# Kernel tuning notes

Measured on AMD Instinct MI355X. Metric: run time of the kernel, lower is better.

The kernel has to match this reference:

```python
import jax, jax.numpy as jnp
import numpy as np


def setup_inputs() -> dict:
    key = jax.random.key(0)
    kq, kk, kv = jax.random.split(key, 3)
    B, N, H, D = 1, 4096, 16, 64
    q = jax.random.normal(kq, (B, N, H, D), dtype=jnp.float32)
    k = jax.random.normal(kk, (B, N, H, D), dtype=jnp.float32)
    v = jax.random.normal(kv, (B, N, H, D), dtype=jnp.float32)
    return {"q": q, "k": k, "v": v}


def reference(q, k, v):
    # q, k, v: [b, n, h, d]
    d = q.shape[-1]
    scale = 1.0 / jnp.sqrt(jnp.asarray(d, dtype=q.dtype))
    # scores: [b, h, n_q, n_k]
    scores = jnp.einsum("bqhd,bkhd->bhqk", q, k) * scale
    attn = jax.nn.softmax(scores, axis=-1)
    # output back in [b, n, h, d] layout
    out = jnp.einsum("bhqk,bkhd->bqhd", attn, v)
    return out
```

## Files before the change

kernel.cpp:

```cpp
#include <hip/hip_runtime.h>
#include <hip/hip_bf16.h>

#define H 16
#define D 64
#define NSEQ 4096
#define BM 128
#define BN 64
#define NT (NSEQ / BN)

typedef __attribute__((ext_vector_type(8))) short bf16x8;
typedef __attribute__((ext_vector_type(4))) short short4v;
typedef __attribute__((ext_vector_type(4))) float f32x4;
typedef __attribute__((ext_vector_type(4))) float f4v;

union BF8 { bf16x8 v; unsigned u[4]; };
union S4  { short4v s; unsigned u[2]; };

static __device__ __forceinline__ unsigned pk2(float lo, float hi) {
    __hip_bfloat162 h = __float22bfloat162_rn(float2{lo, hi});
    unsigned u;
    __builtin_memcpy(&u, &h, 4);
    return u;
}

static __device__ __forceinline__ float fexp2(float x) {
#if __has_builtin(__builtin_amdgcn_exp2f)
    return __builtin_amdgcn_exp2f(x);
#else
    return exp2f(x);
#endif
}

#define TO_GBL(p) ((const __attribute__((address_space(1))) int*)(unsigned long long)(p))
#define TO_LDS(p) ((__attribute__((address_space(3))) int*)(unsigned int)(unsigned long long)(p))

__global__ void prep(const float* __restrict__ k, const float* __restrict__ v,
                     short* __restrict__ kb, short* __restrict__ vt) {
    __shared__ short L[64 * 72];
    const int h = blockIdx.y, n0 = blockIdx.x * 64, t = threadIdx.x;
    const int rw = t >> 4, c4 = (t & 15) * 4;
    #pragma unroll
    for (int it = 0; it < 4; ++it) {
        const int row = rw + it * 16;
        const size_t gro = ((size_t)(n0 + row) * H + h) * D + c4;
        f4v kf = *(const f4v*)(k + gro);
        S4 ks;
        ks.u[0] = pk2(kf[0], kf[1]);
        ks.u[1] = pk2(kf[2], kf[3]);
        *(short4v*)(kb + ((size_t)h * NSEQ + n0 + row) * D + c4) = ks.s;

        f4v vf = *(const f4v*)(v + gro);
        S4 vs;
        vs.u[0] = pk2(vf[0], vf[1]);
        vs.u[1] = pk2(vf[2], vf[3]);
        *(short4v*)&L[row * 72 + c4] = vs.s;
    }
    __syncthreads();
    const int tr = t & 15, tc = t >> 4;
    const int r0 = tr * 4, d0 = tc * 4;
    short4v ra[4];
    #pragma unroll
    for (int i = 0; i < 4; ++i) {
        const int s = r0 + i, s32 = s & 31, base32 = (s >> 5) * 32;
        const int phys = base32 + ((s32 >> 3) * 4 + (s32 & 3) + 16 * ((s32 >> 2) & 1));
        ra[i] = *(const short4v*)&L[phys * 72 + d0];
    }
    #pragma unroll
    for (int jj = 0; jj < 4; ++jj) {
        short4v o4 = (short4v){ra[0][jj], ra[1][jj], ra[2][jj], ra[3][jj]};
        *(short4v*)(vt + ((size_t)(h * D + d0 + jj)) * NSEQ + n0 + r0) = o4;
    }
}

__global__ __launch_bounds__(256, 2)
void attn_fwd(const float* __restrict__ q, const short* __restrict__ kb,
              const short* __restrict__ vtb, float* __restrict__ out)
{
    const int lin   = blockIdx.x;
    const int idx   = lin >> 3;
    const int h     = (lin & 7) * 2 + (idx >> 5);
    const int qbase = (idx & 31) * BM;

    const int tid   = threadIdx.x;
    const int wave  = tid >> 6;
    const int lane  = tid & 63;
    const int lm    = lane & 15;
    const int quad  = lane >> 4;
    const int sw    = lm & 7;

    __shared__ short Kt[4][BN * D];
    __shared__ short Vt[4][BN * D];

    const float c1 = 0.18033688011112042f;

    bf16x8 bq[2][2];
    #pragma unroll
    for (int g = 0; g < 2; ++g) {
        const int qrow = qbase + wave * 32 + g * 16 + lm;
        #pragma unroll
        for (int kc = 0; kc < 2; ++kc) {
            const float* qp = q + ((size_t)qrow * H + h) * D + kc * 32 + quad * 8;
            f4v q0 = *(const f4v*)qp;
            f4v q1 = *(const f4v*)(qp + 4);
            BF8 b;
            b.u[0] = pk2(q0[0] * c1, q0[1] * c1); b.u[1] = pk2(q0[2] * c1, q0[3] * c1);
            b.u[2] = pk2(q1[0] * c1, q1[1] * c1); b.u[3] = pk2(q1[2] * c1, q1[3] * c1);
            bq[g][kc] = b.v;
        }
    }

    BF8 ones;
    ones.u[0] = ones.u[1] = ones.u[2] = ones.u[3] = 0x3F803F80u;

    const f32x4 fz = (f32x4){0.f, 0.f, 0.f, 0.f};
    f32x4 o[2][4];
    #pragma unroll
    for (int g = 0; g < 2; ++g)
        #pragma unroll
        for (int mb = 0; mb < 4; ++mb) o[g][mb] = fz;
    f32x4 lacc[2];
    lacc[0] = fz; lacc[1] = fz;

    const int ci0 = (wave * 2 + 0) * 64 + lane;
    const int ci1 = (wave * 2 + 1) * 64 + lane;
    const int kr0 = ci0 >> 3, kp0 = (ci0 & 7) ^ (kr0 & 7);
    const int kr1 = ci1 >> 3, kp1 = (ci1 & 7) ^ (kr1 & 7);

    const short* kh = kb  + (size_t)h * NSEQ * D;
    const short* vh = vtb + (size_t)h * D * NSEQ;
    const short* pkA = kh + (size_t)kr0 * D + kp0 * 8;
    const short* pkB = kh + (size_t)kr1 * D + kp1 * 8;
    const short* pvA = vh + (size_t)kr0 * NSEQ + kp0 * 8;
    const short* pvB = vh + (size_t)kr1 * NSEQ + kp1 * 8;

    auto issue = [&](int b) {
        __builtin_amdgcn_global_load_lds(TO_GBL(pkA), TO_LDS(&Kt[b][(wave * 2 + 0) * 512]), 16, 0, 0);
        __builtin_amdgcn_global_load_lds(TO_GBL(pkB), TO_LDS(&Kt[b][(wave * 2 + 1) * 512]), 16, 0, 0);
        __builtin_amdgcn_global_load_lds(TO_GBL(pvA), TO_LDS(&Vt[b][(wave * 2 + 0) * 512]), 16, 0, 0);
        __builtin_amdgcn_global_load_lds(TO_GBL(pvB), TO_LDS(&Vt[b][(wave * 2 + 1) * 512]), 16, 0, 0);
        pkA += BN * D; pkB += BN * D; pvA += BN; pvB += BN;
    };

    const int posK0 = ((0 + quad) ^ sw) * 8;
    const int posK1 = ((4 + quad) ^ sw) * 8;

    auto compute = [&](int b) {
        const short* K_ = Kt[b];
        const short* V_ = Vt[b];
        f32x4 st[2][4];

        #pragma unroll
        for (int nb = 0; nb < 4; ++nb) {
            bf16x8 kf0 = *(const bf16x8*)&K_[(nb * 16 + lm) * 64 + posK0];
            bf16x8 kf1 = *(const bf16x8*)&K_[(nb * 16 + lm) * 64 + posK1];
            #pragma unroll
            for (int g = 0; g < 2; ++g) {
                st[g][nb] = __builtin_amdgcn_mfma_f32_16x16x32_bf16(kf0, bq[g][0], fz, 0, 0, 0);
                st[g][nb] = __builtin_amdgcn_mfma_f32_16x16x32_bf16(kf1, bq[g][1], st[g][nb], 0, 0, 0);
            }
        }

        #pragma unroll
        for (int g = 0; g < 2; ++g)
            #pragma unroll
            for (int nb = 0; nb < 4; ++nb)
                #pragma unroll
                for (int r = 0; r < 4; ++r)
                    st[g][nb][r] = fexp2(st[g][nb][r]);

        BF8 pb[2][2];
        #pragma unroll
        for (int g = 0; g < 2; ++g)
            #pragma unroll
            for (int c = 0; c < 2; ++c) {
                pb[g][c].u[0] = pk2(st[g][2 * c][0],     st[g][2 * c][1]);
                pb[g][c].u[1] = pk2(st[g][2 * c][2],     st[g][2 * c][3]);
                pb[g][c].u[2] = pk2(st[g][2 * c + 1][0], st[g][2 * c + 1][1]);
                pb[g][c].u[3] = pk2(st[g][2 * c + 1][2], st[g][2 * c + 1][3]);
            }

        #pragma unroll
        for (int g = 0; g < 2; ++g) {
            lacc[g] = __builtin_amdgcn_mfma_f32_16x16x32_bf16(ones.v, pb[g][0].v, lacc[g], 0, 0, 0);
            lacc[g] = __builtin_amdgcn_mfma_f32_16x16x32_bf16(ones.v, pb[g][1].v, lacc[g], 0, 0, 0);
        }

        #pragma unroll
        for (int c = 0; c < 2; ++c) {
            const int pos = ((c * 4 + quad) ^ sw) * 8;
            #pragma unroll
            for (int mb = 0; mb < 4; ++mb) {
                bf16x8 vf = *(const bf16x8*)&V_[(mb * 16 + lm) * 64 + pos];
                #pragma unroll
                for (int g = 0; g < 2; ++g)
                    o[g][mb] = __builtin_amdgcn_mfma_f32_16x16x32_bf16(vf, pb[g][c].v, o[g][mb], 0, 0, 0);
            }
        }
    };

#define WAITV0 asm volatile("s_waitcnt vmcnt(0)" ::: "memory")
#define BARRIER() do { __builtin_amdgcn_s_barrier(); asm volatile("" ::: "memory"); } while (0)

    issue(0); issue(1);

    for (int k = 0; k < 15; ++k) {
        WAITV0; BARRIER();
        issue(2); issue(3);
        compute(0); compute(1);
        WAITV0; BARRIER();
        issue(0); issue(1);
        compute(2); compute(3);
    }
    WAITV0; BARRIER();
    issue(2); issue(3);
    compute(0); compute(1);
    WAITV0; BARRIER();
    compute(2); compute(3);

    #pragma unroll
    for (int g = 0; g < 2; ++g) {
        const float inv = 1.0f / lacc[g][0];
        const int qrow = qbase + wave * 32 + g * 16 + lm;
        float* op = out + ((size_t)qrow * H + h) * D + quad * 4;
        #pragma unroll
        for (int mb = 0; mb < 4; ++mb) {
            f4v w;
            #pragma unroll
            for (int r = 0; r < 4; ++r) w[r] = o[g][mb][r] * inv;
            *(f4v*)(op + mb * 16) = w;
        }
    }
}

extern "C" void kernel_launch(void* const* d_in, const int* in_sizes, int n_in,
                              void* d_out, int out_size, void* d_ws, size_t ws_size,
                              hipStream_t stream) {
    const float* q = (const float*)d_in[0];
    const float* k = (const float*)d_in[1];
    const float* v = (const float*)d_in[2];
    float* out = (float*)d_out;

    short* kb = (short*)d_ws;
    short* vt = kb + (size_t)H * NSEQ * D;

    prep<<<dim3(NSEQ / 64, H), dim3(256), 0, stream>>>(k, v, kb, vt);
    attn_fwd<<<dim3((NSEQ / BM) * H), dim3(256), 0, stream>>>(q, kb, vt, out);
}
```

Before: 165.7 us.

## Use two waves per block with 64 query rows each for K/V fragment reuse

Shrinks the attention block from four waves to two, so each wave now handles 64 query rows (four 16-row groups) instead of 32. Each K and V fragment read from LDS is reused across twice as many MFMAs, and the K fragments are loaded once per tile up front. Each wave now issues twice as many global-to-LDS loads, the per-thread accumulator and register footprint roughly doubles, and there are fewer waves per block to hide latency. Launch bounds change to 128 threads with a minimum of one block.

After: 179.2 us. 1.08x slower.

```diff
diff --git a/kernel.cpp b/kernel.cpp
--- a/kernel.cpp
+++ b/kernel.cpp
@@ -72,7 +72,7 @@
     }
 }
 
-__global__ __launch_bounds__(256, 2)
+__global__ __launch_bounds__(128, 1)
 void attn_fwd(const float* __restrict__ q, const short* __restrict__ kb,
               const short* __restrict__ vtb, float* __restrict__ out)
 {
@@ -93,10 +93,10 @@
 
     const float c1 = 0.18033688011112042f;
 
-    bf16x8 bq[2][2];
-    #pragma unroll
-    for (int g = 0; g < 2; ++g) {
-        const int qrow = qbase + wave * 32 + g * 16 + lm;
+    bf16x8 bq[4][2];
+    #pragma unroll
+    for (int g = 0; g < 4; ++g) {
+        const int qrow = qbase + wave * 64 + g * 16 + lm;
         #pragma unroll
         for (int kc = 0; kc < 2; ++kc) {
             const float* qp = q + ((size_t)qrow * H + h) * D + kc * 32 + quad * 8;
@@ -113,32 +113,46 @@
     ones.u[0] = ones.u[1] = ones.u[2] = ones.u[3] = 0x3F803F80u;
 
     const f32x4 fz = (f32x4){0.f, 0.f, 0.f, 0.f};
-    f32x4 o[2][4];
-    #pragma unroll
-    for (int g = 0; g < 2; ++g)
+    f32x4 o[4][4];
+    #pragma unroll
+    for (int g = 0; g < 4; ++g)
         #pragma unroll
         for (int mb = 0; mb < 4; ++mb) o[g][mb] = fz;
-    f32x4 lacc[2];
-    lacc[0] = fz; lacc[1] = fz;
-
-    const int ci0 = (wave * 2 + 0) * 64 + lane;
-    const int ci1 = (wave * 2 + 1) * 64 + lane;
-    const int kr0 = ci0 >> 3, kp0 = (ci0 & 7) ^ (kr0 & 7);
-    const int kr1 = ci1 >> 3, kp1 = (ci1 & 7) ^ (kr1 & 7);
+    f32x4 lacc[4];
+    lacc[0] = fz; lacc[1] = fz; lacc[2] = fz; lacc[3] = fz;
+
+    const int cset = wave * 4;
+    const int ciA = (cset + 0) * 64 + lane;
+    const int ciB = (cset + 1) * 64 + lane;
+    const int ciC = (cset + 2) * 64 + lane;
+    const int ciD = (cset + 3) * 64 + lane;
+    const int krA = ciA >> 3, kpA = (ciA & 7) ^ (krA & 7);
+    const int krB = ciB >> 3, kpB = (ciB & 7) ^ (krB & 7);
+    const int krC = ciC >> 3, kpC = (ciC & 7) ^ (krC & 7);
+    const int krD = ciD >> 3, kpD = (ciD & 7) ^ (krD & 7);
 
     const short* kh = kb  + (size_t)h * NSEQ * D;
     const short* vh = vtb + (size_t)h * D * NSEQ;
-    const short* pkA = kh + (size_t)kr0 * D + kp0 * 8;
-    const short* pkB = kh + (size_t)kr1 * D + kp1 * 8;
-    const short* pvA = vh + (size_t)kr0 * NSEQ + kp0 * 8;
-    const short* pvB = vh + (size_t)kr1 * NSEQ + kp1 * 8;
+    const short* pkA = kh + (size_t)krA * D + kpA * 8;
+    const short* pkB = kh + (size_t)krB * D + kpB * 8;
+    const short* pkC = kh + (size_t)krC * D + kpC * 8;
+    const short* pkD = kh + (size_t)krD * D + kpD * 8;
+    const short* pvA = vh + (size_t)krA * NSEQ + kpA * 8;
+    const short* pvB = vh + (size_t)krB * NSEQ + kpB * 8;
+    const short* pvC = vh + (size_t)krC * NSEQ + kpC * 8;
+    const short* pvD = vh + (size_t)krD * NSEQ + kpD * 8;
 
     auto issue = [&](int b) {
-        __builtin_amdgcn_global_load_lds(TO_GBL(pkA), TO_LDS(&Kt[b][(wave * 2 + 0) * 512]), 16, 0, 0);
-        __builtin_amdgcn_global_load_lds(TO_GBL(pkB), TO_LDS(&Kt[b][(wave * 2 + 1) * 512]), 16, 0, 0);
-        __builtin_amdgcn_global_load_lds(TO_GBL(pvA), TO_LDS(&Vt[b][(wave * 2 + 0) * 512]), 16, 0, 0);
-        __builtin_amdgcn_global_load_lds(TO_GBL(pvB), TO_LDS(&Vt[b][(wave * 2 + 1) * 512]), 16, 0, 0);
-        pkA += BN * D; pkB += BN * D; pvA += BN; pvB += BN;
+        __builtin_amdgcn_global_load_lds(TO_GBL(pkA), TO_LDS(&Kt[b][(cset + 0) * 512]), 16, 0, 0);
+        __builtin_amdgcn_global_load_lds(TO_GBL(pkB), TO_LDS(&Kt[b][(cset + 1) * 512]), 16, 0, 0);
+        __builtin_amdgcn_global_load_lds(TO_GBL(pkC), TO_LDS(&Kt[b][(cset + 2) * 512]), 16, 0, 0);
+        __builtin_amdgcn_global_load_lds(TO_GBL(pkD), TO_LDS(&Kt[b][(cset + 3) * 512]), 16, 0, 0);
+        __builtin_amdgcn_global_load_lds(TO_GBL(pvA), TO_LDS(&Vt[b][(cset + 0) * 512]), 16, 0, 0);
+        __builtin_amdgcn_global_load_lds(TO_GBL(pvB), TO_LDS(&Vt[b][(cset + 1) * 512]), 16, 0, 0);
+        __builtin_amdgcn_global_load_lds(TO_GBL(pvC), TO_LDS(&Vt[b][(cset + 2) * 512]), 16, 0, 0);
+        __builtin_amdgcn_global_load_lds(TO_GBL(pvD), TO_LDS(&Vt[b][(cset + 3) * 512]), 16, 0, 0);
+        pkA += BN * D; pkB += BN * D; pkC += BN * D; pkD += BN * D;
+        pvA += BN; pvB += BN; pvC += BN; pvD += BN;
     };
 
     const int posK0 = ((0 + quad) ^ sw) * 8;
@@ -147,43 +161,42 @@
     auto compute = [&](int b) {
         const short* K_ = Kt[b];
         const short* V_ = Vt[b];
-        f32x4 st[2][4];
-
+
+        bf16x8 kf0[4], kf1[4];
         #pragma unroll
         for (int nb = 0; nb < 4; ++nb) {
-            bf16x8 kf0 = *(const bf16x8*)&K_[(nb * 16 + lm) * 64 + posK0];
-            bf16x8 kf1 = *(const bf16x8*)&K_[(nb * 16 + lm) * 64 + posK1];
-            #pragma unroll
-            for (int g = 0; g < 2; ++g) {
-                st[g][nb] = __builtin_amdgcn_mfma_f32_16x16x32_bf16(kf0, bq[g][0], fz, 0, 0, 0);
-                st[g][nb] = __builtin_amdgcn_mfma_f32_16x16x32_bf16(kf1, bq[g][1], st[g][nb], 0, 0, 0);
+            kf0[nb] = *(const bf16x8*)&K_[(nb * 16 + lm) * 64 + posK0];
+            kf1[nb] = *(const bf16x8*)&K_[(nb * 16 + lm) * 64 + posK1];
+        }
+
+        BF8 pb[4][2];
+        #pragma unroll
+        for (int g = 0; g < 4; ++g) {
+            f32x4 st[4];
+            #pragma unroll
+            for (int nb = 0; nb < 4; ++nb) {
+                st[nb] = __builtin_amdgcn_mfma_f32_16x16x32_bf16(kf0[nb], bq[g][0], fz, 0, 0, 0);
+                st[nb] = __builtin_amdgcn_mfma_f32_16x16x32_bf16(kf1[nb], bq[g][1], st[nb], 0, 0, 0);
             }
-        }
-
-        #pragma unroll
-        for (int g = 0; g < 2; ++g)
             #pragma unroll
             for (int nb = 0; nb < 4; ++nb)
                 #pragma unroll
                 for (int r = 0; r < 4; ++r)
-                    st[g][nb][r] = fexp2(st[g][nb][r]);
-
-        BF8 pb[2][2];
-        #pragma unroll
-        for (int g = 0; g < 2; ++g)
+                    st[nb][r] = fexp2(st[nb][r]);
             #pragma unroll
             for (int c = 0; c < 2; ++c) {
-                pb[g][c].u[0] = pk2(st[g][2 * c][0],     st[g][2 * c][1]);
-                pb[g][c].u[1] = pk2(st[g][2 * c][2],     st[g][2 * c][3]);
-                pb[g][c].u[2] = pk2(st[g][2 * c + 1][0], st[g][2 * c + 1][1]);
-                pb[g][c].u[3] = pk2(st[g][2 * c + 1][2], st[g][2 * c + 1][3]);
+                pb[g][c].u[0] = pk2(st[2 * c][0],     st[2 * c][1]);
+                pb[g][c].u[1] = pk2(st[2 * c][2],     st[2 * c][3]);
+                pb[g][c].u[2] = pk2(st[2 * c + 1][0], st[2 * c + 1][1]);
+                pb[g][c].u[3] = pk2(st[2 * c + 1][2], st[2 * c + 1][3]);
             }
-
-        #pragma unroll
-        for (int g = 0; g < 2; ++g) {
-            lacc[g] = __builtin_amdgcn_mfma_f32_16x16x32_bf16(ones.v, pb[g][0].v, lacc[g], 0, 0, 0);
-            lacc[g] = __builtin_amdgcn_mfma_f32_16x16x32_bf16(ones.v, pb[g][1].v, lacc[g], 0, 0, 0);
-        }
+        }
+
+        #pragma unroll
+        for (int c = 0; c < 2; ++c)
+            #pragma unroll
+            for (int g = 0; g < 4; ++g)
+                lacc[g] = __builtin_amdgcn_mfma_f32_16x16x32_bf16(ones.v, pb[g][c].v, lacc[g], 0, 0, 0);
 
         #pragma unroll
         for (int c = 0; c < 2; ++c) {
@@ -192,7 +205,7 @@
             for (int mb = 0; mb < 4; ++mb) {
                 bf16x8 vf = *(const bf16x8*)&V_[(mb * 16 + lm) * 64 + pos];
                 #pragma unroll
-                for (int g = 0; g < 2; ++g)
+                for (int g = 0; g < 4; ++g)
                     o[g][mb] = __builtin_amdgcn_mfma_f32_16x16x32_bf16(vf, pb[g][c].v, o[g][mb], 0, 0, 0);
             }
         }
@@ -218,9 +231,9 @@
     compute(2); compute(3);
 
     #pragma unroll
-    for (int g = 0; g < 2; ++g) {
+    for (int g = 0; g < 4; ++g) {
         const float inv = 1.0f / lacc[g][0];
-        const int qrow = qbase + wave * 32 + g * 16 + lm;
+        const int qrow = qbase + wave * 64 + g * 16 + lm;
         float* op = out + ((size_t)qrow * H + h) * D + quad * 4;
         #pragma unroll
         for (int mb = 0; mb < 4; ++mb) {
@@ -244,5 +257,5 @@
     short* vt = kb + (size_t)H * NSEQ * D;
 
     prep<<<dim3(NSEQ / 64, H), dim3(256), 0, stream>>>(k, v, kb, vt);
-    attn_fwd<<<dim3((NSEQ / BM) * H), dim3(256), 0, stream>>>(q, kb, vt, out);
-}
+    attn_fwd<<<dim3((NSEQ / BM) * H), dim3(128), 0, stream>>>(q, kb, vt, out);
+}
```

## Load K fragments directly from global into double-buffered registers, bypassing LDS

Applied to the files above, without the earlier changes.

K tiles are no longer staged through shared memory with global_load_lds. Each wave now loads its K MFMA fragments straight from global memory into registers, prefetching the next tile while computing on the current one. Only V stays in LDS, which halves shared-memory use and removes the LDS reads for K. In exchange, every wave fetches the full K tile on its own, so L2 traffic for K goes up, the register buffers add VGPR pressure under the 2-blocks-per-CU launch bound, and the vmcnt(0) waits now also cover the K prefetches.

Result: slower. 221.8 us (+33.8%).

```diff
diff --git a/kernel.cpp b/kernel.cpp
--- a/kernel.cpp
+++ b/kernel.cpp
@@ -88,7 +88,6 @@
     const int quad  = lane >> 4;
     const int sw    = lm & 7;
 
-    __shared__ short Kt[4][BN * D];
     __shared__ short Vt[4][BN * D];
 
     const float c1 = 0.18033688011112042f;
@@ -123,40 +122,41 @@
 
     const int ci0 = (wave * 2 + 0) * 64 + lane;
     const int ci1 = (wave * 2 + 1) * 64 + lane;
-    const int kr0 = ci0 >> 3, kp0 = (ci0 & 7) ^ (kr0 & 7);
-    const int kr1 = ci1 >> 3, kp1 = (ci1 & 7) ^ (kr1 & 7);
-
-    const short* kh = kb  + (size_t)h * NSEQ * D;
+    const int vr0 = ci0 >> 3, vp0 = (ci0 & 7) ^ (vr0 & 7);
+    const int vr1 = ci1 >> 3, vp1 = (ci1 & 7) ^ (vr1 & 7);
+
     const short* vh = vtb + (size_t)h * D * NSEQ;
-    const short* pkA = kh + (size_t)kr0 * D + kp0 * 8;
-    const short* pkB = kh + (size_t)kr1 * D + kp1 * 8;
-    const short* pvA = vh + (size_t)kr0 * NSEQ + kp0 * 8;
-    const short* pvB = vh + (size_t)kr1 * NSEQ + kp1 * 8;
+    const short* pvA = vh + (size_t)vr0 * NSEQ + vp0 * 8;
+    const short* pvB = vh + (size_t)vr1 * NSEQ + vp1 * 8;
 
     auto issue = [&](int b) {
-        __builtin_amdgcn_global_load_lds(TO_GBL(pkA), TO_LDS(&Kt[b][(wave * 2 + 0) * 512]), 16, 0, 0);
-        __builtin_amdgcn_global_load_lds(TO_GBL(pkB), TO_LDS(&Kt[b][(wave * 2 + 1) * 512]), 16, 0, 0);
         __builtin_amdgcn_global_load_lds(TO_GBL(pvA), TO_LDS(&Vt[b][(wave * 2 + 0) * 512]), 16, 0, 0);
         __builtin_amdgcn_global_load_lds(TO_GBL(pvB), TO_LDS(&Vt[b][(wave * 2 + 1) * 512]), 16, 0, 0);
-        pkA += BN * D; pkB += BN * D; pvA += BN; pvB += BN;
+        pvA += BN; pvB += BN;
     };
 
-    const int posK0 = ((0 + quad) ^ sw) * 8;
-    const int posK1 = ((4 + quad) ^ sw) * 8;
-
-    auto compute = [&](int b) {
-        const short* K_ = Kt[b];
+    const short* kh = kb + (size_t)h * NSEQ * D;
+    const int krow = lm * D + quad * 8;
+
+    bf16x8 kA0[4], kA1[4], kB0[4], kB1[4];
+    auto loadK = [&](const short* kt, bf16x8* f0, bf16x8* f1) {
+        #pragma unroll
+        for (int nb = 0; nb < 4; ++nb) {
+            f0[nb] = *(const bf16x8*)&kt[nb * 16 * D + krow];
+            f1[nb] = *(const bf16x8*)&kt[nb * 16 * D + krow + 32];
+        }
+    };
+
+    auto compute = [&](int b, const bf16x8* kf0, const bf16x8* kf1) {
         const short* V_ = Vt[b];
         f32x4 st[2][4];
 
         #pragma unroll
         for (int nb = 0; nb < 4; ++nb) {
-            bf16x8 kf0 = *(const bf16x8*)&K_[(nb * 16 + lm) * 64 + posK0];
-            bf16x8 kf1 = *(const bf16x8*)&K_[(nb * 16 + lm) * 64 + posK1];
             #pragma unroll
             for (int g = 0; g < 2; ++g) {
-                st[g][nb] = __builtin_amdgcn_mfma_f32_16x16x32_bf16(kf0, bq[g][0], fz, 0, 0, 0);
-                st[g][nb] = __builtin_amdgcn_mfma_f32_16x16x32_bf16(kf1, bq[g][1], st[g][nb], 0, 0, 0);
+                st[g][nb] = __builtin_amdgcn_mfma_f32_16x16x32_bf16(kf0[nb], bq[g][0], fz, 0, 0, 0);
+                st[g][nb] = __builtin_amdgcn_mfma_f32_16x16x32_bf16(kf1[nb], bq[g][1], st[g][nb], 0, 0, 0);
             }
         }
 
@@ -202,20 +202,37 @@
 #define BARRIER() do { __builtin_amdgcn_s_barrier(); asm volatile("" ::: "memory"); } while (0)
 
     issue(0); issue(1);
+    loadK(kh, kA0, kA1);
+    const short* kc1 = kh + BN * D;
 
     for (int k = 0; k < 15; ++k) {
         WAITV0; BARRIER();
         issue(2); issue(3);
-        compute(0); compute(1);
+        loadK(kc1, kB0, kB1);
+        compute(0, kA0, kA1);
+        loadK(kc1 + BN * D, kA0, kA1);
+        compute(1, kB0, kB1);
+        kc1 += 2 * BN * D;
+
         WAITV0; BARRIER();
         issue(0); issue(1);
-        compute(2); compute(3);
+        loadK(kc1, kB0, kB1);
+        compute(2, kA0, kA1);
+        loadK(kc1 + BN * D, kA0, kA1);
+        compute(3, kB0, kB1);
+        kc1 += 2 * BN * D;
     }
     WAITV0; BARRIER();
     issue(2); issue(3);
-    compute(0); compute(1);
+    loadK(kc1, kB0, kB1);
+    compute(0, kA0, kA1);
+    loadK(kc1 + BN * D, kA0, kA1);
+    compute(1, kB0, kB1);
+    kc1 += 2 * BN * D;
     WAITV0; BARRIER();
-    compute(2); compute(3);
+    loadK(kc1, kB0, kB1);
+    compute(2, kA0, kA1);
+    compute(3, kB0, kB1);
 
     #pragma unroll
     for (int g = 0; g < 2; ++g) {
```
